# Kernel tuning notes

Measured on AMD Instinct MI355X. Metric: run time of the kernel, lower is better.

The kernel has to match this reference:

```python
import jax, jax.numpy as jnp
import numpy as np

M = 4096
N = 4096


def precompute_expk(n):
    # Twiddle factors exp(-i*pi*k/(2n)), k = 0..n-1 (matches DREAMPlace precompute_expk)
    k = jnp.arange(n)
    return jnp.exp(-1j * jnp.pi * k.astype(jnp.float32) / (2.0 * n)).astype(jnp.complex64)


def setup_inputs() -> dict:
    key = jax.random.key(0)
    x = jax.random.normal(key, (M, N), dtype=jnp.float32)
    return {"x": x, "expkM": precompute_expk(M), "expkN": precompute_expk(N)}


def _dct1d(x, expk):
    """DCT-II along the last axis via Makhoul's even/odd reorder + FFT + twiddle.

    y[k] = sum_n x[n] * cos(pi * (2n+1) * k / (2L))  (unnormalized, no factor 2)
    """
    # reorder: even-indexed samples forward, odd-indexed samples reversed
    v = jnp.concatenate([x[..., 0::2], x[..., 1::2][..., ::-1]], axis=-1)
    V = jnp.fft.fft(v, axis=-1)
    return jnp.real(V * expk)


def reference(x, expkM, expkN):
    # 2D DCT-II: transform columns (length N), then rows (length M)
    y = _dct1d(x, expkN)            # [M, N], DCT along axis -1
    y = _dct1d(y.T, expkM).T        # DCT along axis 0
    return y
```

## Files before the change

kernel.cpp:

```cpp
#include <hip/hip_runtime.h>
#include <hip/hip_bf16.h>


#define L 4096

__device__ __forceinline__ int SWZ(int e) {
    return e ^ (((e >> 4) ^ (e >> 8)) & 15);
}

__device__ __forceinline__ float2 cmul(float2 a, float2 b) {
    return make_float2(a.x * b.x - a.y * b.y, a.x * b.y + a.y * b.x);
}

__device__ __forceinline__ void bfly4(float2& x0, float2& x1, float2& x2, float2& x3) {
    float t0x = x0.x + x2.x, t0y = x0.y + x2.y;
    float t1x = x0.x - x2.x, t1y = x0.y - x2.y;
    float t2x = x1.x + x3.x, t2y = x1.y + x3.y;
    float t3x = x1.x - x3.x, t3y = x1.y - x3.y;
    x0 = make_float2(t0x + t2x, t0y + t2y);
    x1 = make_float2(t1x + t3y, t1y - t3x);
    x2 = make_float2(t0x - t2x, t0y - t2y);
    x3 = make_float2(t1x - t3y, t1y + t3x);
}

#define FOR8(X) X(0) X(1) X(2) X(3) X(4) X(5) X(6) X(7)

#define FFT8N(P) \
  bfly4(P##0, P##2, P##4, P##6); \
  bfly4(P##1, P##3, P##5, P##7); \
  { float2 e1_=P##2, e2_=P##4, e3_=P##6, o0_=P##1, o1_=P##3, o2_=P##5, o3_=P##7; \
    o1_ = cmul(o1_, make_float2(0.70710678118654752f, -0.70710678118654752f)); \
    o2_ = make_float2(o2_.y, -o2_.x); \
    o3_ = cmul(o3_, make_float2(-0.70710678118654752f, -0.70710678118654752f)); \
    float2 e0_=P##0; \
    P##0 = make_float2(e0_.x+o0_.x, e0_.y+o0_.y); \
    P##4 = make_float2(e0_.x-o0_.x, e0_.y-o0_.y); \
    P##1 = make_float2(e1_.x+o1_.x, e1_.y+o1_.y); \
    P##5 = make_float2(e1_.x-o1_.x, e1_.y-o1_.y); \
    P##2 = make_float2(e2_.x+o2_.x, e2_.y+o2_.y); \
    P##6 = make_float2(e2_.x-o2_.x, e2_.y-o2_.y); \
    P##3 = make_float2(e3_.x+o3_.x, e3_.y+o3_.y); \
    P##7 = make_float2(e3_.x-o3_.x, e3_.y-o3_.y); }

#define TWCHAIN(P, W) { float2 f_ = W; \
    P##1 = cmul(P##1, f_); f_ = cmul(f_, W); \
    P##2 = cmul(P##2, f_); f_ = cmul(f_, W); \
    P##3 = cmul(P##3, f_); f_ = cmul(f_, W); \
    P##4 = cmul(P##4, f_); f_ = cmul(f_, W); \
    P##5 = cmul(P##5, f_); f_ = cmul(f_, W); \
    P##6 = cmul(P##6, f_); f_ = cmul(f_, W); \
    P##7 = cmul(P##7, f_); }


template <int Q>
__device__ __forceinline__ void stage_pair(float2* lds, int t) {
    const int j = t & (Q - 1);
    const int G = t / Q;
    const int base = G * 16 * Q + j;

    float2 v[4][4];
#pragma unroll
    for (int b = 0; b < 4; ++b)
#pragma unroll
        for (int a = 0; a < 4; ++a)
            v[a][b] = lds[SWZ(base + (a + 4 * b) * Q)];

    if (Q > 1) {
        float c1, s1;
        __sincosf((float)j * (-6.2831853071795864769f / (4.0f * (float)Q)), &s1, &c1);
        float2 w1 = make_float2(c1, s1);
        float2 w2 = cmul(w1, w1);
        float2 w3 = cmul(w2, w1);
#pragma unroll
        for (int b = 0; b < 4; ++b) {
            v[1][b] = cmul(v[1][b], w1);
            v[2][b] = cmul(v[2][b], w2);
            v[3][b] = cmul(v[3][b], w3);
        }
    }
#pragma unroll
    for (int b = 0; b < 4; ++b) bfly4(v[0][b], v[1][b], v[2][b], v[3][b]);

    float2 u;
    if (Q == 1) {
        u = make_float2(1.0f, 0.0f);
    } else {
        float cu, su;
        __sincosf((float)j * (-6.2831853071795864769f / (16.0f * (float)Q)), &su, &cu);
        u = make_float2(cu, su);
    }
    const float2 E = make_float2(0.92387953251128674f, -0.38268343236508977f);
    float2 w = u;
#pragma unroll
    for (int a = 0; a < 4; ++a) {
        if (!(Q == 1 && a == 0)) {
            float2 W2 = cmul(w, w);
            float2 W3 = cmul(W2, w);
            v[a][1] = cmul(v[a][1], w);
            v[a][2] = cmul(v[a][2], W2);
            v[a][3] = cmul(v[a][3], W3);
        }
        bfly4(v[a][0], v[a][1], v[a][2], v[a][3]);
        if (a < 3) w = cmul(w, E);
    }

#pragma unroll
    for (int b = 0; b < 4; ++b)
#pragma unroll
        for (int a = 0; a < 4; ++a)
            lds[SWZ(base + (a + 4 * b) * Q)] = v[a][b];
}

__global__ __launch_bounds__(256)
void dct_rows2_kernel(const float* __restrict__ in, float* __restrict__ out) {
    __shared__ float2 lds[L];

    const int r0 = blockIdx.x * 2;
    const int t = threadIdx.x;
    const float* rowA = in + (size_t)r0 * L;
    const float* rowB = rowA + L;

    const int revT4 = ((t & 3) << 6) | ((t & 12) << 2) | ((t >> 2) & 12) | ((t >> 6) & 3);

#pragma unroll
    for (int w = 0; w < 8; ++w) {
        int n = w * 256 + t;
        float2 fa = *reinterpret_cast<const float2*>(&rowA[2 * n]);
        float2 fb = *reinterpret_cast<const float2*>(&rowB[2 * n]);
        int p = (revT4 << 4) | ((w & 3) << 2) | (w >> 2);
        lds[SWZ(p)]        = make_float2(fa.x, fb.x);
        lds[SWZ(4095 - p)] = make_float2(fa.y, fb.y);
    }
    __syncthreads();

    stage_pair<1>(lds, t);
    __syncthreads();
    stage_pair<16>(lds, t);
    __syncthreads();
    stage_pair<256>(lds, t);
    __syncthreads();

    float* outA = out + (size_t)r0 * L;
    float* outB = outA + L;

    float2 e;
    __sincosf((float)t * 3.8349519697141029e-4f, &e.y, &e.x);
    const float2 ST = make_float2(0.99518472667219693f, 0.09801714032956060f);
#pragma unroll
    for (int w = 0; w < 16; ++w) {
        int k = w * 256 + t;
        float2 Zk = lds[SWZ(k)];
        int m = (L - k) & (L - 1);
        float2 Zm = lds[SWZ(m)];

        float vax = 0.5f * (Zk.x + Zm.x);
        float vay = 0.5f * (Zk.y - Zm.y);
        float vbx = 0.5f * (Zk.y + Zm.y);
        float vby = 0.5f * (Zm.x - Zk.x);

        outA[k] = vax * e.x + vay * e.y;
        outB[k] = vbx * e.x + vby * e.y;
        e = cmul(e, ST);
    }
}

__global__ __launch_bounds__(512)
void fft64_col_a2(const float* __restrict__ Y, float* __restrict__ ws) {
    __shared__ float2 xch[4096];
    const int c = threadIdx.x & 63;
    const int v = threadIdx.x >> 6;
    const int b = blockIdx.x;
    const int T = blockIdx.y;
    const int ca = T * 128 + c;
    const int cb = ca + 64;

#define LDA(u) float2 g##u; { \
        const int aa = 8 * u + v; \
        const int row = (u < 4) ? (128 * aa + 2 * b) : (8191 - 128 * aa - 2 * b); \
        const float* rp = Y + (size_t)row * L; \
        g##u = make_float2(rp[ca], rp[cb]); }
    FOR8(LDA)
#undef LDA

    FFT8N(g)

#define WRA(t) xch[v * 512 + t * 64 + c] = g##t;
    FOR8(WRA)
#undef WRA
    __syncthreads();
#define RDA(vv) g##vv = xch[vv * 512 + v * 64 + c];
    FOR8(RDA)
#undef RDA

    float2 wv; __sincosf((float)v * -0.09817477042468103f, &wv.y, &wv.x);
    TWCHAIN(g, wv)

    FFT8N(g)

    float2 mw, ms;
    __sincosf((float)(b * v) * -1.5339807878856412e-3f, &mw.y, &mw.x);
    __sincosf((float)b * -1.2271846303085130e-2f, &ms.y, &ms.x);
    float2* wp = reinterpret_cast<float2*>(ws) + (size_t)b * 2048 + (size_t)T * 64 + c;
#define STA(s) { \
        g##s = cmul(g##s, mw); \
        wp[(size_t)(8 * s + v) * 131072] = g##s; \
        mw = cmul(mw, ms); }
    FOR8(STA)
#undef STA
}

__global__ __launch_bounds__(512)
void fft64_col_b3(const float* __restrict__ wsf, float* __restrict__ out) {
    __shared__ float2 xch[8192];
    const int c  = threadIdx.x & 63;
    const int v  = threadIdx.x >> 6;
    const int qa = blockIdx.x;
    const int T  = blockIdx.y;
    const int q  = qa;
    const int q2 = (qa == 0) ? 32 : 64 - qa;

    const float2* wsc = reinterpret_cast<const float2*>(wsf);
    const size_t cbase = (size_t)T * 64 + c;

#define LDH(u) \
    float2 ha##u = wsc[(size_t)q  * 131072 + (size_t)(8*u+v) * 2048 + cbase]; \
    float2 hp##u = wsc[(size_t)q2 * 131072 + (size_t)(8*u+v) * 2048 + cbase];
    FOR8(LDH)
#undef LDH

    float2 wv; __sincosf((float)v * -0.09817477042468103f, &wv.y, &wv.x);

    FFT8N(ha)
#define W1(k) xch[v * 512 + k * 64 + c] = ha##k;
    FOR8(W1)
#undef W1
    __syncthreads();
#define DECLG(i) float2 g##i;
    FOR8(DECLG)
#undef DECLG
#define R1(vv) g##vv = xch[vv * 512 + v * 64 + c];
    FOR8(R1)
#undef R1
    TWCHAIN(g, wv)
    FFT8N(g)

#define SV(a) float2 gq##a = g##a; xch[4096 + (8*a + v) * 64 + c] = g##a;
    FOR8(SV)
#undef SV
    __syncthreads();

    FFT8N(hp)
#define W2(k) xch[v * 512 + k * 64 + c] = hp##k;
    FOR8(W2)
#undef W2
    __syncthreads();
#define R2(vv) g##vv = xch[vv * 512 + v * 64 + c];
    FOR8(R2)
#undef R2
    TWCHAIN(g, wv)
    FFT8N(g)
    __syncthreads();
#define W3(a) xch[(8*a + v) * 64 + c] = g##a;
    FOR8(W3)
#undef W3
    __syncthreads();

    const float2 STEP = make_float2(0.98078528040323045f, 0.19509032201612827f);
    float2 eq, eq2;
    __sincosf((float)(64 * v + q ) * 3.8349519697141029e-4f, &eq.y,  &eq.x);
    __sincosf((float)(64 * v + q2) * 3.8349519697141029e-4f, &eq2.y, &eq2.x);
    const int colA = T * 128 + c;

#define CMB(a) { \
    const int p_ = 8 * a + v; \
    float2 rq  = (qa == 0) ? xch[4096 + (((64 - p_) & 63) * 64) + c] \
                           : xch[(63 - p_) * 64 + c]; \
    float2 rq2 = (qa == 0) ? xch[(63 - p_) * 64 + c] \
                           : xch[4096 + (63 - p_) * 64 + c]; \
    float FAx = 0.5f * (gq##a.x + rq.x), FAy = 0.5f * (gq##a.y - rq.y); \
    float FBx = 0.5f * (gq##a.y + rq.y), FBy = 0.5f * (rq.x - gq##a.x); \
    size_t rowq = (size_t)(512 * a + 64 * v + q) * L; \
    out[rowq + colA]      = FAx * eq.x + FAy * eq.y; \
    out[rowq + colA + 64] = FBx * eq.x + FBy * eq.y; \
    float GAx = 0.5f * (g##a.x + rq2.x), GAy = 0.5f * (g##a.y - rq2.y); \
    float GBx = 0.5f * (g##a.y + rq2.y), GBy = 0.5f * (rq2.x - g##a.x); \
    size_t rowq2 = (size_t)(512 * a + 64 * v + q2) * L; \
    out[rowq2 + colA]      = GAx * eq2.x + GAy * eq2.y; \
    out[rowq2 + colA + 64] = GBx * eq2.x + GBy * eq2.y; \
    eq = cmul(eq, STEP); eq2 = cmul(eq2, STEP); }
    FOR8(CMB)
#undef CMB
}

extern "C" void kernel_launch(void* const* d_in, const int* in_sizes, int n_in,
                              void* d_out, int out_size, void* d_ws, size_t ws_size,
                              hipStream_t stream) {
    const float* x = (const float*)d_in[0];
    float* out = (float*)d_out;
    float* ws  = (float*)d_ws;

    dct_rows2_kernel<<<L / 2, 256, 0, stream>>>(x, out);
    fft64_col_a2<<<dim3(64, 32), 512, 0, stream>>>(out, ws);
    fft64_col_b3<<<dim3(32, 32), 512, 0, stream>>>(ws, out);
}
```

Before: 79.95 us.

## Rewrite row DCT kernel as 512-thread 64x64 four-step FFT with padded LDS

Replaces the 256-thread radix-16 stage-pair row FFT with a 512-thread four-step decomposition (8x8 subFFTs in registers, 64-point transposes through padded shared memory, inter-stage twiddles). Each thread now holds 8 complex values instead of 16, and the swizzle function is dropped in favour of padding. The aim is higher occupancy and less LDS index arithmetic. The cost is more barriers and more shared-memory exchange passes. Macro names in the column kernel are renamed to avoid clashes.

```diff
diff --git a/kernel.cpp b/kernel.cpp
--- a/kernel.cpp
+++ b/kernel.cpp
@@ -3,10 +3,6 @@
 
 
 #define L 4096
-
-__device__ __forceinline__ int SWZ(int e) {
-    return e ^ (((e >> 4) ^ (e >> 8)) & 15);
-}
 
 __device__ __forceinline__ float2 cmul(float2 a, float2 b) {
     return make_float2(a.x * b.x - a.y * b.y, a.x * b.y + a.y * b.x);
@@ -23,6 +19,7 @@
     x3 = make_float2(t1x - t3y, t1y + t3x);
 }
 
+#define FOR4(X) X(0) X(1) X(2) X(3)
 #define FOR8(X) X(0) X(1) X(2) X(3) X(4) X(5) X(6) X(7)
 
 #define FFT8N(P) \
@@ -51,118 +48,91 @@
     P##6 = cmul(P##6, f_); f_ = cmul(f_, W); \
     P##7 = cmul(P##7, f_); }
 
-
-template <int Q>
-__device__ __forceinline__ void stage_pair(float2* lds, int t) {
-    const int j = t & (Q - 1);
-    const int G = t / Q;
-    const int base = G * 16 * Q + j;
-
-    float2 v[4][4];
-#pragma unroll
-    for (int b = 0; b < 4; ++b)
-#pragma unroll
-        for (int a = 0; a < 4; ++a)
-            v[a][b] = lds[SWZ(base + (a + 4 * b) * Q)];
-
-    if (Q > 1) {
-        float c1, s1;
-        __sincosf((float)j * (-6.2831853071795864769f / (4.0f * (float)Q)), &s1, &c1);
-        float2 w1 = make_float2(c1, s1);
-        float2 w2 = cmul(w1, w1);
-        float2 w3 = cmul(w2, w1);
-#pragma unroll
-        for (int b = 0; b < 4; ++b) {
-            v[1][b] = cmul(v[1][b], w1);
-            v[2][b] = cmul(v[2][b], w2);
-            v[3][b] = cmul(v[3][b], w3);
-        }
-    }
-#pragma unroll
-    for (int b = 0; b < 4; ++b) bfly4(v[0][b], v[1][b], v[2][b], v[3][b]);
-
-    float2 u;
-    if (Q == 1) {
-        u = make_float2(1.0f, 0.0f);
-    } else {
-        float cu, su;
-        __sincosf((float)j * (-6.2831853071795864769f / (16.0f * (float)Q)), &su, &cu);
-        u = make_float2(cu, su);
-    }
-    const float2 E = make_float2(0.92387953251128674f, -0.38268343236508977f);
-    float2 w = u;
-#pragma unroll
-    for (int a = 0; a < 4; ++a) {
-        if (!(Q == 1 && a == 0)) {
-            float2 W2 = cmul(w, w);
-            float2 W3 = cmul(W2, w);
-            v[a][1] = cmul(v[a][1], w);
-            v[a][2] = cmul(v[a][2], W2);
-            v[a][3] = cmul(v[a][3], W3);
-        }
-        bfly4(v[a][0], v[a][1], v[a][2], v[a][3]);
-        if (a < 3) w = cmul(w, E);
-    }
-
-#pragma unroll
-    for (int b = 0; b < 4; ++b)
-#pragma unroll
-        for (int a = 0; a < 4; ++a)
-            lds[SWZ(base + (a + 4 * b) * Q)] = v[a][b];
-}
-
-__global__ __launch_bounds__(256)
-void dct_rows2_kernel(const float* __restrict__ in, float* __restrict__ out) {
-    __shared__ float2 lds[L];
-
+__global__ __launch_bounds__(512)
+void dct_rows4_kernel(const float* __restrict__ in, float* __restrict__ out) {
+    __shared__ float2 xch[4160];
+    const int l = threadIdx.x & 63;
+    const int v = threadIdx.x >> 6;
     const int r0 = blockIdx.x * 2;
-    const int t = threadIdx.x;
     const float* rowA = in + (size_t)r0 * L;
     const float* rowB = rowA + L;
 
-    const int revT4 = ((t & 3) << 6) | ((t & 12) << 2) | ((t >> 2) & 12) | ((t >> 6) & 3);
-
-#pragma unroll
-    for (int w = 0; w < 8; ++w) {
-        int n = w * 256 + t;
-        float2 fa = *reinterpret_cast<const float2*>(&rowA[2 * n]);
-        float2 fb = *reinterpret_cast<const float2*>(&rowB[2 * n]);
-        int p = (revT4 << 4) | ((w & 3) << 2) | (w >> 2);
-        lds[SWZ(p)]        = make_float2(fa.x, fb.x);
-        lds[SWZ(4095 - p)] = make_float2(fa.y, fb.y);
-    }
-    __syncthreads();
-
-    stage_pair<1>(lds, t);
-    __syncthreads();
-    stage_pair<16>(lds, t);
-    __syncthreads();
-    stage_pair<256>(lds, t);
+#define LD1(u) { \
+        const int n = 512*u + 64*v + l; \
+        float2 fa = *reinterpret_cast<const float2*>(&rowA[2*n]); \
+        float2 fb = *reinterpret_cast<const float2*>(&rowB[2*n]); \
+        xch[n]        = make_float2(fa.x, fb.x); \
+        xch[4095 - n] = make_float2(fa.y, fb.y); }
+    FOR4(LD1)
+#undef LD1
+    __syncthreads();
+#define R1(u) float2 g##u = xch[512*u + 64*v + l];
+    FOR8(R1)
+#undef R1
+    __syncthreads();
+
+    FFT8N(g)
+#define W2(t) xch[512*v + 64*t + l] = g##t;
+    FOR8(W2)
+#undef W2
+    __syncthreads();
+#define R2(vv) g##vv = xch[512*vv + 64*v + l];
+    FOR8(R2)
+#undef R2
+    __syncthreads();
+
+    float2 wv; __sincosf((float)v * -0.09817477042468103f, &wv.y, &wv.x);
+    TWCHAIN(g, wv)
+    FFT8N(g)
+
+    float2 mw, ms;
+    __sincosf((float)(l * v) * -1.5339807878856412e-3f, &mw.y, &mw.x);
+    __sincosf((float)l * -1.2271846303085130e-2f, &ms.y, &ms.x);
+#define W3(s) { g##s = cmul(g##s, mw); xch[520*s + 65*v + l] = g##s; mw = cmul(mw, ms); }
+    FOR8(W3)
+#undef W3
+    __syncthreads();
+#define R3(u) g##u = xch[65*l + 8*u + v];
+    FOR8(R3)
+#undef R3
+    __syncthreads();
+
+    FFT8N(g)
+#define W4(t) xch[512*v + 64*t + l] = g##t;
+    FOR8(W4)
+#undef W4
+    __syncthreads();
+#define R4(vv) g##vv = xch[512*vv + 64*v + l];
+    FOR8(R4)
+#undef R4
+    __syncthreads();
+
+    TWCHAIN(g, wv)
+    FFT8N(g)
+
+#define W5(s) xch[520*s + 65*v + l] = g##s;
+    FOR8(W5)
+#undef W5
     __syncthreads();
 
     float* outA = out + (size_t)r0 * L;
     float* outB = outA + L;
-
-    float2 e;
-    __sincosf((float)t * 3.8349519697141029e-4f, &e.y, &e.x);
-    const float2 ST = make_float2(0.99518472667219693f, 0.09801714032956060f);
-#pragma unroll
-    for (int w = 0; w < 16; ++w) {
-        int k = w * 256 + t;
-        float2 Zk = lds[SWZ(k)];
-        int m = (L - k) & (L - 1);
-        float2 Zm = lds[SWZ(m)];
-
-        float vax = 0.5f * (Zk.x + Zm.x);
-        float vay = 0.5f * (Zk.y - Zm.y);
-        float vbx = 0.5f * (Zk.y + Zm.y);
-        float vby = 0.5f * (Zm.x - Zk.x);
-
-        outA[k] = vax * e.x + vay * e.y;
-        outB[k] = vbx * e.x + vby * e.y;
-        e = cmul(e, ST);
-    }
-}
+    float2 e; __sincosf((float)(64*v + l) * 3.8349519697141029e-4f, &e.y, &e.x);
+    const float2 ST = make_float2(0.98078528040323045f, 0.19509032201612827f);
+#define EP5(s) { \
+        const int k = 512*s + 64*v + l; \
+        const int m = (4096 - k) & 4095; \
+        float2 Zk = g##s; \
+        float2 Zm = xch[(m >> 6) * 65 + (m & 63)]; \
+        float vax = 0.5f*(Zk.x + Zm.x), vay = 0.5f*(Zk.y - Zm.y); \
+        float vbx = 0.5f*(Zk.y + Zm.y), vby = 0.5f*(Zm.x - Zk.x); \
+        outA[k] = vax*e.x + vay*e.y; \
+        outB[k] = vbx*e.x + vby*e.y; \
+        e = cmul(e, ST); }
+    FOR8(EP5)
+#undef EP5
+}
+
 
 __global__ __launch_bounds__(512)
 void fft64_col_a2(const float* __restrict__ Y, float* __restrict__ ws) {
@@ -238,9 +208,9 @@
 #define DECLG(i) float2 g##i;
     FOR8(DECLG)
 #undef DECLG
-#define R1(vv) g##vv = xch[vv * 512 + v * 64 + c];
-    FOR8(R1)
-#undef R1
+#define R1b(vv) g##vv = xch[vv * 512 + v * 64 + c];
+    FOR8(R1b)
+#undef R1b
     TWCHAIN(g, wv)
     FFT8N(g)
 
@@ -250,19 +220,19 @@
     __syncthreads();
 
     FFT8N(hp)
-#define W2(k) xch[v * 512 + k * 64 + c] = hp##k;
-    FOR8(W2)
-#undef W2
-    __syncthreads();
-#define R2(vv) g##vv = xch[vv * 512 + v * 64 + c];
-    FOR8(R2)
-#undef R2
-    TWCHAIN(g, wv)
-    FFT8N(g)
-    __syncthreads();
-#define W3(a) xch[(8*a + v) * 64 + c] = g##a;
-    FOR8(W3)
-#undef W3
+#define W2b(k) xch[v * 512 + k * 64 + c] = hp##k;
+    FOR8(W2b)
+#undef W2b
+    __syncthreads();
+#define R2b(vv) g##vv = xch[vv * 512 + v * 64 + c];
+    FOR8(R2b)
+#undef R2b
+    TWCHAIN(g, wv)
+    FFT8N(g)
+    __syncthreads();
+#define W3b(a) xch[(8*a + v) * 64 + c] = g##a;
+    FOR8(W3b)
+#undef W3b
     __syncthreads();
 
     const float2 STEP = make_float2(0.98078528040323045f, 0.19509032201612827f);
@@ -299,7 +269,7 @@
     float* out = (float*)d_out;
     float* ws  = (float*)d_ws;
 
-    dct_rows2_kernel<<<L / 2, 256, 0, stream>>>(x, out);
+    dct_rows4_kernel<<<L / 2, 512, 0, stream>>>(x, out);
     fft64_col_a2<<<dim3(64, 32), 512, 0, stream>>>(out, ws);
     fft64_col_b3<<<dim3(32, 32), 512, 0, stream>>>(ws, out);
 }
```

New measurement: 72.41 us. 9.4% less time.
